# Optimization experiments

Hardware: AMD Instinct MI355X
Metric: run time of the kernel (lower is better)

Reference implementation:

```python
import jax, jax.numpy as jnp
import numpy as np

N_NODES = 100000
N_EDGES = 1600000
IN_DIM = 3
LATENT = 128
LATENT_DEC = 128
NUM_LAYER = 2      # shared-weight middle GCN layers
NUM_LAYER_DEC = 2  # shared-weight middle decoder layers


def _glorot(key, shape):
    fan_in, fan_out = shape[0], shape[1]
    lim = np.sqrt(6.0 / (fan_in + fan_out)).astype(np.float32)
    return jax.random.uniform(key, shape, jnp.float32, -lim, lim)


def setup_inputs() -> dict:
    key = jax.random.key(0)
    ks = jax.random.split(key, 10)
    x = jax.random.normal(ks[0], (N_NODES, IN_DIM), jnp.float32)
    edge_index = jax.random.randint(ks[1], (2, N_EDGES), 0, N_NODES, jnp.int64)
    return {
        "x": x,
        "edge_index": edge_index,
        "W_s": _glorot(ks[2], (IN_DIM, LATENT)),   "b_s": jnp.zeros((LATENT,), jnp.float32),
        "W_m": _glorot(ks[3], (LATENT, LATENT)),   "b_m": jnp.zeros((LATENT,), jnp.float32),
        "W_e": _glorot(ks[4], (LATENT, LATENT)),   "b_e": jnp.zeros((LATENT,), jnp.float32),
        "W_sd": _glorot(ks[5], (LATENT, LATENT_DEC)),    "b_sd": jnp.zeros((LATENT_DEC,), jnp.float32),
        "W_md": _glorot(ks[6], (LATENT_DEC, LATENT_DEC)),"b_md": jnp.zeros((LATENT_DEC,), jnp.float32),
        "W_ed": _glorot(ks[7], (LATENT_DEC, IN_DIM)),    "b_ed": jnp.zeros((IN_DIM,), jnp.float32),
    }


def _gcn_conv(h, W, b, src, dst, dinv):
    # PyG GCNConv: out_i = sum_j norm_ij * (x_j @ W) + b, norm = d^-1/2_i d^-1/2_j
    h = h @ W
    norm = dinv[src] * dinv[dst]                       # [E+N]
    msg = norm[:, None] * h[src]                       # gather + scale
    out = jax.ops.segment_sum(msg, dst, num_segments=N_NODES)  # scatter-add
    return out + b


def reference(x, edge_index, W_s, b_s, W_m, b_m, W_e, b_e, W_sd, b_sd, W_md, b_md, W_ed, b_ed):
    loops = jnp.arange(N_NODES, dtype=edge_index.dtype)
    src = jnp.concatenate([edge_index[0], loops])      # add self-loops
    dst = jnp.concatenate([edge_index[1], loops])
    deg = jax.ops.segment_sum(jnp.ones(src.shape[0], x.dtype), dst, num_segments=N_NODES)
    dinv = jnp.where(deg > 0, jax.lax.rsqrt(deg), 0.0)

    h = jax.nn.relu(_gcn_conv(x, W_s, b_s, src, dst, dinv))
    for _ in range(NUM_LAYER):  # shared weights (ModuleList([layer]*n))
        h = jax.nn.relu(_gcn_conv(h, W_m, b_m, src, dst, dinv))
    h = jax.nn.relu(_gcn_conv(h, W_e, b_e, src, dst, dinv))

    h = jax.nn.relu(h @ W_sd + b_sd)
    for _ in range(NUM_LAYER_DEC):  # shared weights
        h = jax.nn.relu(h @ W_md + b_md)
    y = h @ W_ed + b_ed
    return y + x
```

## Files before the change

### kernel.cpp

```cpp
#include <hip/hip_runtime.h>


typedef __attribute__((ext_vector_type(8))) short short8;
typedef __attribute__((ext_vector_type(4))) float floatx4;
typedef __attribute__((ext_vector_type(2))) float floatx2;

#define BIN_CH 8192
#define NBMAX 512
#define BKT 256
#define HS_STRIDE 68

__device__ __forceinline__ unsigned short f2bf(float f) {
    unsigned int u = __float_as_uint(f);
    u += 0x7fffu + ((u >> 16) & 1u);
    return (unsigned short)(u >> 16);
}
__device__ __forceinline__ unsigned int pk_bf(float a, float b) {
    return (unsigned int)f2bf(a) | ((unsigned int)f2bf(b) << 16);
}
__device__ __forceinline__ unsigned char f2fp8(float f) {
    return (unsigned char)(__builtin_amdgcn_cvt_pk_fp8_f32(f, f, 0, false) & 0xFF);
}
__device__ __forceinline__ short8 ld_frag(const unsigned short* p) {
    uint2 a = *(const uint2*)p;
    uint2 b = *(const uint2*)(p + 4);
    int4 v = make_int4((int)a.x, (int)a.y, (int)b.x, (int)b.y);
    return __builtin_bit_cast(short8, v);
}


__global__ void pack_kernel(const float* __restrict__ W0, const float* __restrict__ W1,
                            const float* __restrict__ W2, const float* __restrict__ W3,
                            unsigned short* __restrict__ P0, unsigned short* __restrict__ P1,
                            unsigned short* __restrict__ P2, unsigned short* __restrict__ P3,
                            int* __restrict__ gfill, unsigned char* __restrict__ t8zrowA,
                            unsigned char* __restrict__ t8zrowB, int NB) {
    if (blockIdx.x == 0) {
        for (int i = threadIdx.x; i < NB; i += 256) gfill[i] = 0;
        if (threadIdx.x < 32) {
            ((unsigned int*)t8zrowA)[threadIdx.x] = 0;
            ((unsigned int*)t8zrowB)[threadIdx.x] = 0;
        }
    }
    int which = blockIdx.x >> 3;
    const float* W = which == 0 ? W0 : which == 1 ? W1 : which == 2 ? W2 : W3;
    unsigned short* P = which == 0 ? P0 : which == 1 ? P1 : which == 2 ? P2 : P3;
    int f = (blockIdx.x & 7) * 256 + threadIdx.x;
    int lane = f & 63, nt = (f >> 6) & 7, kc = f >> 9;
    int kbase = kc * 32 + (lane >> 4) * 8;
    int ncol = nt * 16 + (lane & 15);
    short8 frag;
    #pragma unroll
    for (int j = 0; j < 8; ++j)
        frag[j] = (short)f2bf(W[(size_t)(kbase + j) * 128 + ncol]);
    *((short8*)(P + (size_t)f * 8)) = frag;
}


__global__ __launch_bounds__(512) void bin_kernel(
        const int* __restrict__ src, const int* __restrict__ dst,
        int* __restrict__ gfill, unsigned int* __restrict__ binbuf,
        int NB, int C, int E) {
    __shared__ int h4[4][NBMAX];
    __shared__ int start[NBMAX];
    __shared__ int tot[NBMAX];
    __shared__ int dstoff[NBMAX];
    int tid = threadIdx.x;
    int grp = tid >> 7;
    int e0 = blockIdx.x * BIN_CH;
    for (int i = tid; i < 4 * NBMAX; i += 512) ((int*)h4)[i] = 0;
    __syncthreads();
    for (int i = tid; i < BIN_CH; i += 512) {
        int e = e0 + i;
        if (e < E) atomicAdd(&h4[grp][dst[e] >> 8], 1);
    }
    __syncthreads();
    if (tid < 64) {
        int carry = 0;
        for (int base = 0; base < NB; base += 64) {
            int idx = base + tid;
            int c0 = 0, c1 = 0, c2 = 0, c3 = 0, v = 0;
            if (idx < NB) {
                c0 = h4[0][idx]; c1 = h4[1][idx];
                c2 = h4[2][idx]; c3 = h4[3][idx];
                v = c0 + c1 + c2 + c3;
            }
            int s = v;
            #pragma unroll
            for (int off = 1; off < 64; off <<= 1) {
                int u = __shfl_up(s, off);
                if (tid >= off) s += u;
            }
            if (idx < NB) {
                int ex = carry + s - v;
                start[idx] = ex;
                tot[idx] = v;
                h4[0][idx] = ex;
                h4[1][idx] = ex + c0;
                h4[2][idx] = ex + c0 + c1;
                h4[3][idx] = ex + c0 + c1 + c2;
            }
            carry += __shfl(s, 63);
        }
    }
    __syncthreads();
    for (int i = tid; i < NB; i += 512) {
        int cnt = tot[i];
        int g = cnt ? atomicAdd(&gfill[i], cnt) : 0;
        dstoff[i] = g - start[i];
    }
    __syncthreads();
    for (int i = tid; i < BIN_CH; i += 512) {
        int e = e0 + i;
        if (e >= E) continue;
        int d = dst[e];
        int b = d >> 8;
        int slot = atomicAdd(&h4[grp][b], 1);
        int gidx = b * C + dstoff[b] + slot;
        if (gidx < (b + 1) * C)
            binbuf[gidx] = (unsigned int)src[e] | ((unsigned int)(d & 255) << 17);
    }
}

__global__ __launch_bounds__(256) void build_kernel(
        const unsigned int* __restrict__ binbuf, const int* __restrict__ gfill,
        int* __restrict__ rowptr, float* __restrict__ dinv, int* __restrict__ col,
        int NB, int C, int N, int E) {
    __shared__ int h4[4][BKT];
    __shared__ int hs[BKT];
    __shared__ int tot[BKT];
    __shared__ int bbase_s;
    int b = blockIdx.x, tid = threadIdx.x;
    int grp = tid >> 6;
    int cnt = gfill[b];
    const unsigned int* p = binbuf + (size_t)b * C;
    for (int i = tid; i < 4 * BKT; i += 256) ((int*)h4)[i] = 0;
    __syncthreads();
    if (tid >= 64 && tid < 128) {
        int l = tid - 64;
        int s = 0;
        for (int i = l; i < b; i += 64) s += gfill[i];
        #pragma unroll
        for (int off = 32; off > 0; off >>= 1) s += __shfl_down(s, off);
        if (l == 0) bbase_s = s;
    }
    for (int i = tid; i < cnt; i += 256) atomicAdd(&h4[grp][p[i] >> 17], 1);
    __syncthreads();
    if (tid < 64) {
        int carry = 0;
        for (int base = 0; base < BKT; base += 64) {
            int idx = base + tid;
            int c0 = h4[0][idx], c1 = h4[1][idx], c2 = h4[2][idx], c3 = h4[3][idx];
            int v = c0 + c1 + c2 + c3;
            int s = v;
            #pragma unroll
            for (int off = 1; off < 64; off <<= 1) {
                int u = __shfl_up(s, off);
                if (tid >= off) s += u;
            }
            int ex = carry + s - v;
            hs[idx] = ex;
            tot[idx] = v;
            h4[0][idx] = ex;
            h4[1][idx] = ex + c0;
            h4[2][idx] = ex + c0 + c1;
            h4[3][idx] = ex + c0 + c1 + c2;
            carry += __shfl(s, 63);
        }
    }
    __syncthreads();
    int base = bbase_s;
    if (tid < BKT) {
        int node = b * BKT + tid;
        if (node < N) {
            rowptr[node] = base + hs[tid];
            dinv[node] = 1.0f / sqrtf((float)(tot[tid] + 1));
        }
    }
    if (b == 0 && tid == 0) rowptr[N] = E;
    __syncthreads();
    for (int i = tid; i < cnt; i += 256) {
        unsigned int u = p[i];
        int local = u >> 17;
        int pos = atomicAdd(&h4[grp][local], 1);
        col[base + pos] = (int)(u & 0x1FFFFu);
    }
}


__global__ void in_gemm_kernel(const float* __restrict__ x, const float* __restrict__ W,
                               const float* __restrict__ dinv,
                               unsigned char* __restrict__ t8, int n) {
    int g = blockIdx.x * 256 + threadIdx.x;
    int i = g >> 6, c2 = g & 63;
    if (i >= n) return;
    float x0 = x[i * 3], x1 = x[i * 3 + 1], x2 = x[i * 3 + 2];
    float d = dinv[i];
    int c = c2 * 2;
    float v0 = d * (x0 * W[c]     + x1 * W[128 + c]     + x2 * W[256 + c]);
    float v1 = d * (x0 * W[c + 1] + x1 * W[128 + c + 1] + x2 * W[256 + c + 1]);
    unsigned int pk = __builtin_amdgcn_cvt_pk_fp8_f32(v0, v1, 0, false);
    ((unsigned short*)t8)[(size_t)i * 64 + c2] = (unsigned short)(pk & 0xFFFF);
}


__device__ __forceinline__ void gemm_regs(const short8 af[2][4], const unsigned short* Ws,
                                          int lane, floatx4 acc[2][8]) {
    #pragma unroll
    for (int t = 0; t < 2; ++t)
        #pragma unroll
        for (int nt = 0; nt < 8; ++nt) acc[t][nt] = (floatx4){0.f, 0.f, 0.f, 0.f};
    #pragma unroll
    for (int kc = 0; kc < 4; ++kc) {
        #pragma unroll
        for (int nt = 0; nt < 8; ++nt) {
            short8 bf = *((const short8*)(Ws + ((kc * 8 + nt) * 64 + lane) * 8));
            acc[0][nt] = __builtin_amdgcn_mfma_f32_16x16x32_bf16(af[0][kc], bf, acc[0][nt], 0, 0, 0);
            acc[1][nt] = __builtin_amdgcn_mfma_f32_16x16x32_bf16(af[1][kc], bf, acc[1][nt], 0, 0, 0);
        }
    }
}

__device__ __forceinline__ void gemm_lds(const unsigned short* Hs, const unsigned short* Ws,
                                         int wav, int lane, floatx4 acc[2][8]) {
    int quad = lane >> 4, mrow = lane & 15;
    short8 af[2][4];
    #pragma unroll
    for (int t = 0; t < 2; ++t)
        #pragma unroll
        for (int kc = 0; kc < 4; ++kc)
            af[t][kc] = ld_frag(Hs + (wav * 32 + t * 16 + mrow) * HS_STRIDE + (kc * 4 + quad) * 8);
    gemm_regs(af, Ws, lane, acc);
}

__device__ __forceinline__ void relu_store_hs(
        unsigned short* Hs, const float* __restrict__ bias,
        floatx4 acc[2][8], int wav, int lane) {
    int quad = lane >> 4, mrow = lane & 15;
    #pragma unroll
    for (int t = 0; t < 2; ++t) {
        #pragma unroll
        for (int nt = 0; nt < 8; ++nt) {
            int colc = nt * 16 + mrow;
            float bcol = bias[colc];
            #pragma unroll
            for (int r = 0; r < 4; ++r) {
                int rowl = wav * 32 + t * 16 + quad * 4 + r;
                Hs[rowl * HS_STRIDE + colc] = f2bf(fmaxf(acc[t][nt][r] + bcol, 0.f));
            }
        }
    }
}


__device__ __forceinline__ void agg_to_hs(
        const unsigned char* __restrict__ t8, const int* __restrict__ rowptr,
        const int* __restrict__ col, const float* __restrict__ dinv,
        const float* __restrict__ bias, unsigned short* Hs, int n) {
    int tid = threadIdx.x;
    int lane = tid & 63;
    int q16 = lane >> 4;
    int lq  = lane & 15;
    int oct = (lane >> 3) & 1;
    int l8  = lane & 7;
    int qrow0 = (tid >> 4) * 8;
    const float4* b4 = (const float4*)bias;

    for (int it = 0; it < 8; ++it) {
        int rowl = qrow0 + it;
        int node = blockIdx.x * 128 + rowl;
        if (node >= n) node = n - 1;
        floatx2 acc[8];
        #pragma unroll
        for (int i = 0; i < 8; ++i) acc[i] = (floatx2){0.f, 0.f};

        int beg = rowptr[node];
        int deg = rowptr[node + 1] - beg;
        for (int base = 0; base < deg; base += 32) {
            int m = deg - base;
            int jv0 = (lq < m)      ? col[beg + base + lq]      : n;
            int jv1 = (lq + 16 < m) ? col[beg + base + 16 + lq] : n;
            uint4 v[16];
            #pragma unroll
            for (int q = 0; q < 8; ++q) {
                int j = __shfl(jv0, q16 * 16 + q * 2 + oct);
                v[q] = ((const uint4*)(t8 + (size_t)j * 128))[l8];
            }
            #pragma unroll
            for (int q = 0; q < 8; ++q) {
                int j = __shfl(jv1, q16 * 16 + q * 2 + oct);
                v[8 + q] = ((const uint4*)(t8 + (size_t)j * 128))[l8];
            }
            #pragma unroll
            for (int q = 0; q < 16; ++q) {
                acc[0] += __builtin_amdgcn_cvt_pk_f32_fp8(v[q].x, false);
                acc[1] += __builtin_amdgcn_cvt_pk_f32_fp8(v[q].x, true);
                acc[2] += __builtin_amdgcn_cvt_pk_f32_fp8(v[q].y, false);
                acc[3] += __builtin_amdgcn_cvt_pk_f32_fp8(v[q].y, true);
                acc[4] += __builtin_amdgcn_cvt_pk_f32_fp8(v[q].z, false);
                acc[5] += __builtin_amdgcn_cvt_pk_f32_fp8(v[q].z, true);
                acc[6] += __builtin_amdgcn_cvt_pk_f32_fp8(v[q].w, false);
                acc[7] += __builtin_amdgcn_cvt_pk_f32_fp8(v[q].w, true);
            }
        }
        #pragma unroll
        for (int i = 0; i < 8; ++i) {
            acc[i].x += __shfl_xor(acc[i].x, 8);
            acc[i].y += __shfl_xor(acc[i].y, 8);
        }
        uint4 s = ((const uint4*)(t8 + (size_t)node * 128))[l8];
        acc[0] += __builtin_amdgcn_cvt_pk_f32_fp8(s.x, false);
        acc[1] += __builtin_amdgcn_cvt_pk_f32_fp8(s.x, true);
        acc[2] += __builtin_amdgcn_cvt_pk_f32_fp8(s.y, false);
        acc[3] += __builtin_amdgcn_cvt_pk_f32_fp8(s.y, true);
        acc[4] += __builtin_amdgcn_cvt_pk_f32_fp8(s.z, false);
        acc[5] += __builtin_amdgcn_cvt_pk_f32_fp8(s.z, true);
        acc[6] += __builtin_amdgcn_cvt_pk_f32_fp8(s.w, false);
        acc[7] += __builtin_amdgcn_cvt_pk_f32_fp8(s.w, true);

        float di = dinv[node];
        float o[16];
        #pragma unroll
        for (int k = 0; k < 4; ++k) {
            float4 bb = b4[l8 * 4 + k];
            o[k*4+0] = fmaxf(di * acc[k*2].x   + bb.x, 0.f);
            o[k*4+1] = fmaxf(di * acc[k*2].y   + bb.y, 0.f);
            o[k*4+2] = fmaxf(di * acc[k*2+1].x + bb.z, 0.f);
            o[k*4+3] = fmaxf(di * acc[k*2+1].y + bb.w, 0.f);
        }
        if (oct == 0) {
            unsigned short* hp = Hs + rowl * HS_STRIDE + l8 * 16;
            uint2 w;
            w.x = pk_bf(o[0],  o[1]);  w.y = pk_bf(o[2],  o[3]);
            *(uint2*)(hp)     = w;
            w.x = pk_bf(o[4],  o[5]);  w.y = pk_bf(o[6],  o[7]);
            *(uint2*)(hp + 4) = w;
            w.x = pk_bf(o[8],  o[9]);  w.y = pk_bf(o[10], o[11]);
            *(uint2*)(hp + 8) = w;
            w.x = pk_bf(o[12], o[13]); w.y = pk_bf(o[14], o[15]);
            *(uint2*)(hp + 12) = w;
        }
    }
}


__global__ __launch_bounds__(256, 3) void agg_gemm_kernel(
        const unsigned char* __restrict__ t8, const int* __restrict__ rowptr,
        const int* __restrict__ col, const float* __restrict__ dinv,
        const float* __restrict__ bias, const unsigned short* __restrict__ Wp,
        unsigned char* __restrict__ outp, int n) {
    __shared__ unsigned short Hs[128 * HS_STRIDE];
    agg_to_hs(t8, rowptr, col, dinv, bias, Hs, n);

    int tid = threadIdx.x;
    int wav = tid >> 6, lane = tid & 63;
    int quad = lane >> 4, mrow = lane & 15;
    int row0 = blockIdx.x * 128 + wav * 32;

    floatx4 acc[2][8];
    gemm_lds(Hs, Wp, wav, lane, acc);

    #pragma unroll
    for (int t = 0; t < 2; ++t) {
        int rbase = row0 + t * 16 + quad * 4;
        float dv[4];
        #pragma unroll
        for (int r = 0; r < 4; ++r)
            dv[r] = (rbase + r < n) ? dinv[rbase + r] : 0.f;
        #pragma unroll
        for (int nt = 0; nt < 8; ++nt) {
            int colc = nt * 16 + mrow;
            #pragma unroll
            for (int r = 0; r < 4; ++r) {
                int row = rbase + r;
                if (row < n)
                    outp[(size_t)row * 128 + colc] = f2fp8(acc[t][nt][r] * dv[r]);
            }
        }
    }
}


__global__ __launch_bounds__(256, 3) void agg_dec_kernel(
        const unsigned char* __restrict__ t8, const int* __restrict__ rowptr,
        const int* __restrict__ col, const float* __restrict__ dinv,
        const float* __restrict__ bias,
        const unsigned short* __restrict__ Wp_sd, const float* __restrict__ b_sd,
        const unsigned short* __restrict__ Wp_md, const float* __restrict__ b_md,
        const float* __restrict__ W_ed, const float* __restrict__ b_ed,
        const float* __restrict__ x, float* __restrict__ out, int n) {
    __shared__ unsigned short Hs[128 * HS_STRIDE];
    agg_to_hs(t8, rowptr, col, dinv, bias, Hs, n);

    int tid = threadIdx.x;
    int wav = tid >> 6, lane = tid & 63;
    int quad = lane >> 4, mrow = lane & 15;
    int row0 = blockIdx.x * 128 + wav * 32;

    floatx4 acc[2][8];
    gemm_lds(Hs, Wp_sd, wav, lane, acc);
    relu_store_hs(Hs, b_sd, acc, wav, lane);
    gemm_lds(Hs, Wp_md, wav, lane, acc);
    relu_store_hs(Hs, b_md, acc, wav, lane);
    gemm_lds(Hs, Wp_md, wav, lane, acc);

    float wed[8][3];
    #pragma unroll
    for (int nt = 0; nt < 8; ++nt) {
        int c = nt * 16 + mrow;
        #pragma unroll
        for (int k = 0; k < 3; ++k) wed[nt][k] = W_ed[c * 3 + k];
    }
    #pragma unroll
    for (int t = 0; t < 2; ++t) {
        #pragma unroll
        for (int r = 0; r < 4; ++r) {
            float s0 = 0.f, s1 = 0.f, s2 = 0.f;
            #pragma unroll
            for (int nt = 0; nt < 8; ++nt) {
                float v = fmaxf(acc[t][nt][r] + b_md[nt * 16 + mrow], 0.f);
                s0 += v * wed[nt][0]; s1 += v * wed[nt][1]; s2 += v * wed[nt][2];
            }
            #pragma unroll
            for (int off = 1; off < 16; off <<= 1) {
                s0 += __shfl_xor(s0, off);
                s1 += __shfl_xor(s1, off);
                s2 += __shfl_xor(s2, off);
            }
            if (mrow == 0) {
                int row = row0 + t * 16 + quad * 4 + r;
                if (row < n) {
                    out[row * 3 + 0] = s0 + b_ed[0] + x[row * 3 + 0];
                    out[row * 3 + 1] = s1 + b_ed[1] + x[row * 3 + 1];
                    out[row * 3 + 2] = s2 + b_ed[2] + x[row * 3 + 2];
                }
            }
        }
    }
}


extern "C" void kernel_launch(void* const* d_in, const int* in_sizes, int n_in,
                              void* d_out, int out_size, void* d_ws, size_t ws_size,
                              hipStream_t stream) {
    const float* x    = (const float*)d_in[0];
    const int*   ei   = (const int*)d_in[1];
    const float* W_s  = (const float*)d_in[2];
    const float* b_s  = (const float*)d_in[3];
    const float* W_m  = (const float*)d_in[4];
    const float* b_m  = (const float*)d_in[5];
    const float* W_e  = (const float*)d_in[6];
    const float* b_e  = (const float*)d_in[7];
    const float* W_sd = (const float*)d_in[8];
    const float* b_sd = (const float*)d_in[9];
    const float* W_md = (const float*)d_in[10];
    const float* b_md = (const float*)d_in[11];
    const float* W_ed = (const float*)d_in[12];
    const float* b_ed = (const float*)d_in[13];
    float* outp = (float*)d_out;

    const int N = in_sizes[0] / 3;
    const int E = in_sizes[1] / 2;
    const int* src = ei;
    const int* dst = ei + E;

    const int NB = (N + BKT - 1) / BKT;
    const int C  = (((E / NB) * 3 / 2) + 255) & ~255;

    char* p = (char*)d_ws;
    auto carve = [&](size_t bytes) {
        void* r = (void*)p;
        p += (bytes + 255) & ~(size_t)255;
        return r;
    };
    int*   rowptr = (int*)  carve((size_t)(N + 1) * 4);
    int*   col    = (int*)  carve((size_t)E * 4);
    float* dinv   = (float*)carve((size_t)N * 4);
    int*   gfill  = (int*)  carve((size_t)NB * 4);
    unsigned int* binbuf = (unsigned int*)carve((size_t)NB * C * 4);
    unsigned short* Wp_m  = (unsigned short*)carve(16384 * 2);
    unsigned short* Wp_e  = (unsigned short*)carve(16384 * 2);
    unsigned short* Wp_sd = (unsigned short*)carve(16384 * 2);
    unsigned short* Wp_md = (unsigned short*)carve(16384 * 2);
    unsigned char*  T8a = (unsigned char*) carve((size_t)(N + 1) * 128);
    unsigned char*  T8b = (unsigned char*) carve((size_t)(N + 1) * 128);
    (void)ws_size;

    const int gBin = (E + BIN_CH - 1) / BIN_CH;
    const int gRow128 = (N + 127) / 128;

    pack_kernel<<<32, 256, 0, stream>>>(W_m, W_e, W_sd, W_md, Wp_m, Wp_e, Wp_sd, Wp_md,
                                        gfill, T8a + (size_t)N * 128,
                                        T8b + (size_t)N * 128, NB);

    bin_kernel<<<gBin, 512, 0, stream>>>(src, dst, gfill, binbuf, NB, C, E);
    build_kernel<<<NB, 256, 0, stream>>>(binbuf, gfill, rowptr, dinv, col, NB, C, N, E);

    in_gemm_kernel<<<(N * 64 + 255) / 256, 256, 0, stream>>>(x, W_s, dinv, T8a, N);
    agg_gemm_kernel<<<gRow128, 256, 0, stream>>>(T8a, rowptr, col, dinv, b_s, Wp_m, T8b, N);
    agg_gemm_kernel<<<gRow128, 256, 0, stream>>>(T8b, rowptr, col, dinv, b_m, Wp_m, T8a, N);
    agg_gemm_kernel<<<gRow128, 256, 0, stream>>>(T8a, rowptr, col, dinv, b_m, Wp_e, T8b, N);

    agg_dec_kernel<<<gRow128, 256, 0, stream>>>(T8b, rowptr, col, dinv, b_e,
                                                Wp_sd, b_sd, Wp_md, b_md,
                                                W_ed, b_ed, x, outp, N);
}
```

Baseline: 372.9 us.

## Use 512-thread blocks and prefetch next node's neighbor indices during aggregation

Blocks grow from 256 to 512 threads, so each wave handles 16 rows of the MFMA GEMM instead of 32 and each thread group aggregates 4 nodes instead of 8. The aggregation loop now loads rowptr for all of its nodes up front, issues the self-loop feature load early, and fetches the next node's column indices while the current node's gathers are in flight. Launch bounds move to (512,4). The goal is more waves per CU and better hiding of gather latency, at the cost of register pressure and a second MFMA pass per row tile being lost.

```diff
diff --git a/kernel.cpp b/kernel.cpp
--- a/kernel.cpp
+++ b/kernel.cpp
@@ -204,50 +204,42 @@
 }
 
 
-__device__ __forceinline__ void gemm_regs(const short8 af[2][4], const unsigned short* Ws,
-                                          int lane, floatx4 acc[2][8]) {
-    #pragma unroll
-    for (int t = 0; t < 2; ++t)
-        #pragma unroll
-        for (int nt = 0; nt < 8; ++nt) acc[t][nt] = (floatx4){0.f, 0.f, 0.f, 0.f};
+__device__ __forceinline__ void gemm_regs16(const short8 af[4], const unsigned short* Ws,
+                                            int lane, floatx4 acc[8]) {
+    #pragma unroll
+    for (int nt = 0; nt < 8; ++nt) acc[nt] = (floatx4){0.f, 0.f, 0.f, 0.f};
     #pragma unroll
     for (int kc = 0; kc < 4; ++kc) {
         #pragma unroll
         for (int nt = 0; nt < 8; ++nt) {
             short8 bf = *((const short8*)(Ws + ((kc * 8 + nt) * 64 + lane) * 8));
-            acc[0][nt] = __builtin_amdgcn_mfma_f32_16x16x32_bf16(af[0][kc], bf, acc[0][nt], 0, 0, 0);
-            acc[1][nt] = __builtin_amdgcn_mfma_f32_16x16x32_bf16(af[1][kc], bf, acc[1][nt], 0, 0, 0);
-        }
-    }
-}
-
-__device__ __forceinline__ void gemm_lds(const unsigned short* Hs, const unsigned short* Ws,
-                                         int wav, int lane, floatx4 acc[2][8]) {
+            acc[nt] = __builtin_amdgcn_mfma_f32_16x16x32_bf16(af[kc], bf, acc[nt], 0, 0, 0);
+        }
+    }
+}
+
+__device__ __forceinline__ void gemm_lds16(const unsigned short* Hs, const unsigned short* Ws,
+                                           int wav, int lane, floatx4 acc[8]) {
     int quad = lane >> 4, mrow = lane & 15;
-    short8 af[2][4];
-    #pragma unroll
-    for (int t = 0; t < 2; ++t)
-        #pragma unroll
-        for (int kc = 0; kc < 4; ++kc)
-            af[t][kc] = ld_frag(Hs + (wav * 32 + t * 16 + mrow) * HS_STRIDE + (kc * 4 + quad) * 8);
-    gemm_regs(af, Ws, lane, acc);
-}
-
-__device__ __forceinline__ void relu_store_hs(
+    short8 af[4];
+    #pragma unroll
+    for (int kc = 0; kc < 4; ++kc)
+        af[kc] = ld_frag(Hs + (wav * 16 + mrow) * HS_STRIDE + (kc * 4 + quad) * 8);
+    gemm_regs16(af, Ws, lane, acc);
+}
+
+__device__ __forceinline__ void relu_store_hs16(
         unsigned short* Hs, const float* __restrict__ bias,
-        floatx4 acc[2][8], int wav, int lane) {
+        floatx4 acc[8], int wav, int lane) {
     int quad = lane >> 4, mrow = lane & 15;
     #pragma unroll
-    for (int t = 0; t < 2; ++t) {
-        #pragma unroll
-        for (int nt = 0; nt < 8; ++nt) {
-            int colc = nt * 16 + mrow;
-            float bcol = bias[colc];
-            #pragma unroll
-            for (int r = 0; r < 4; ++r) {
-                int rowl = wav * 32 + t * 16 + quad * 4 + r;
-                Hs[rowl * HS_STRIDE + colc] = f2bf(fmaxf(acc[t][nt][r] + bcol, 0.f));
-            }
+    for (int nt = 0; nt < 8; ++nt) {
+        int colc = nt * 16 + mrow;
+        float bcol = bias[colc];
+        #pragma unroll
+        for (int r = 0; r < 4; ++r) {
+            int rowl = wav * 16 + quad * 4 + r;
+            Hs[rowl * HS_STRIDE + colc] = f2bf(fmaxf(acc[nt][r] + bcol, 0.f));
         }
     }
 }
@@ -263,32 +255,69 @@
     int lq  = lane & 15;
     int oct = (lane >> 3) & 1;
     int l8  = lane & 7;
-    int qrow0 = (tid >> 4) * 8;
+    int qrow0 = (tid >> 4) * 4;
     const float4* b4 = (const float4*)bias;
 
-    for (int it = 0; it < 8; ++it) {
+    int nd0 = blockIdx.x * 128 + qrow0;
+    int bg[4], dg[4];
+    #pragma unroll
+    for (int it = 0; it < 4; ++it) {
+        int node = nd0 + it; if (node >= n) node = n - 1;
+        bg[it] = rowptr[node];
+        dg[it] = rowptr[node + 1] - bg[it];
+    }
+    int jv0 = (lq < dg[0])      ? col[bg[0] + lq]      : n;
+    int jv1 = (lq + 16 < dg[0]) ? col[bg[0] + 16 + lq] : n;
+
+    for (int it = 0; it < 4; ++it) {
         int rowl = qrow0 + it;
-        int node = blockIdx.x * 128 + rowl;
-        if (node >= n) node = n - 1;
+        int node = nd0 + it; if (node >= n) node = n - 1;
         floatx2 acc[8];
         #pragma unroll
         for (int i = 0; i < 8; ++i) acc[i] = (floatx2){0.f, 0.f};
 
-        int beg = rowptr[node];
-        int deg = rowptr[node + 1] - beg;
-        for (int base = 0; base < deg; base += 32) {
+        uint4 s = ((const uint4*)(t8 + (size_t)node * 128))[l8];
+
+        int deg = dg[it];
+        uint4 v[16];
+        #pragma unroll
+        for (int q = 0; q < 8; ++q) {
+            int j = __shfl(jv0, q16 * 16 + q * 2 + oct);
+            v[q] = ((const uint4*)(t8 + (size_t)j * 128))[l8];
+        }
+        #pragma unroll
+        for (int q = 0; q < 8; ++q) {
+            int j = __shfl(jv1, q16 * 16 + q * 2 + oct);
+            v[8 + q] = ((const uint4*)(t8 + (size_t)j * 128))[l8];
+        }
+        int njv0 = n, njv1 = n;
+        if (it < 3) {
+            njv0 = (lq < dg[it + 1])      ? col[bg[it + 1] + lq]      : n;
+            njv1 = (lq + 16 < dg[it + 1]) ? col[bg[it + 1] + 16 + lq] : n;
+        }
+        #pragma unroll
+        for (int q = 0; q < 16; ++q) {
+            acc[0] += __builtin_amdgcn_cvt_pk_f32_fp8(v[q].x, false);
+            acc[1] += __builtin_amdgcn_cvt_pk_f32_fp8(v[q].x, true);
+            acc[2] += __builtin_amdgcn_cvt_pk_f32_fp8(v[q].y, false);
+            acc[3] += __builtin_amdgcn_cvt_pk_f32_fp8(v[q].y, true);
+            acc[4] += __builtin_amdgcn_cvt_pk_f32_fp8(v[q].z, false);
+            acc[5] += __builtin_amdgcn_cvt_pk_f32_fp8(v[q].z, true);
+            acc[6] += __builtin_amdgcn_cvt_pk_f32_fp8(v[q].w, false);
+            acc[7] += __builtin_amdgcn_cvt_pk_f32_fp8(v[q].w, true);
+        }
+        for (int base = 32; base < deg; base += 32) {
             int m = deg - base;
-            int jv0 = (lq < m)      ? col[beg + base + lq]      : n;
-            int jv1 = (lq + 16 < m) ? col[beg + base + 16 + lq] : n;
-            uint4 v[16];
+            int a0 = (lq < m)      ? col[bg[it] + base + lq]      : n;
+            int a1 = (lq + 16 < m) ? col[bg[it] + base + 16 + lq] : n;
             #pragma unroll
             for (int q = 0; q < 8; ++q) {
-                int j = __shfl(jv0, q16 * 16 + q * 2 + oct);
+                int j = __shfl(a0, q16 * 16 + q * 2 + oct);
                 v[q] = ((const uint4*)(t8 + (size_t)j * 128))[l8];
             }
             #pragma unroll
             for (int q = 0; q < 8; ++q) {
-                int j = __shfl(jv1, q16 * 16 + q * 2 + oct);
+                int j = __shfl(a1, q16 * 16 + q * 2 + oct);
                 v[8 + q] = ((const uint4*)(t8 + (size_t)j * 128))[l8];
             }
             #pragma unroll
@@ -308,7 +337,6 @@
             acc[i].x += __shfl_xor(acc[i].x, 8);
             acc[i].y += __shfl_xor(acc[i].y, 8);
         }
-        uint4 s = ((const uint4*)(t8 + (size_t)node * 128))[l8];
         acc[0] += __builtin_amdgcn_cvt_pk_f32_fp8(s.x, false);
         acc[1] += __builtin_amdgcn_cvt_pk_f32_fp8(s.x, true);
         acc[2] += __builtin_amdgcn_cvt_pk_f32_fp8(s.y, false);
@@ -332,19 +360,20 @@
             unsigned short* hp = Hs + rowl * HS_STRIDE + l8 * 16;
             uint2 w;
             w.x = pk_bf(o[0],  o[1]);  w.y = pk_bf(o[2],  o[3]);
-            *(uint2*)(hp)     = w;
+            *(uint2*)(hp)      = w;
             w.x = pk_bf(o[4],  o[5]);  w.y = pk_bf(o[6],  o[7]);
-            *(uint2*)(hp + 4) = w;
+            *(uint2*)(hp + 4)  = w;
             w.x = pk_bf(o[8],  o[9]);  w.y = pk_bf(o[10], o[11]);
-            *(uint2*)(hp + 8) = w;
+            *(uint2*)(hp + 8)  = w;
             w.x = pk_bf(o[12], o[13]); w.y = pk_bf(o[14], o[15]);
             *(uint2*)(hp + 12) = w;
         }
-    }
-}
-
-
-__global__ __launch_bounds__(256, 3) void agg_gemm_kernel(
+        jv0 = njv0; jv1 = njv1;
+    }
+}
+
+
+__global__ __launch_bounds__(512, 4) void agg_gemm_kernel(
         const unsigned char* __restrict__ t8, const int* __restrict__ rowptr,
         const int* __restrict__ col, const float* __restrict__ dinv,
         const float* __restrict__ bias, const unsigned short* __restrict__ Wp,
@@ -355,33 +384,30 @@
     int tid = threadIdx.x;
     int wav = tid >> 6, lane = tid & 63;
     int quad = lane >> 4, mrow = lane & 15;
-    int row0 = blockIdx.x * 128 + wav * 32;
-
-    floatx4 acc[2][8];
-    gemm_lds(Hs, Wp, wav, lane, acc);
-
-    #pragma unroll
-    for (int t = 0; t < 2; ++t) {
-        int rbase = row0 + t * 16 + quad * 4;
-        float dv[4];
-        #pragma unroll
-        for (int r = 0; r < 4; ++r)
-            dv[r] = (rbase + r < n) ? dinv[rbase + r] : 0.f;
-        #pragma unroll
-        for (int nt = 0; nt < 8; ++nt) {
-            int colc = nt * 16 + mrow;
-            #pragma unroll
-            for (int r = 0; r < 4; ++r) {
-                int row = rbase + r;
-                if (row < n)
-                    outp[(size_t)row * 128 + colc] = f2fp8(acc[t][nt][r] * dv[r]);
-            }
-        }
-    }
-}
-
-
-__global__ __launch_bounds__(256, 3) void agg_dec_kernel(
+    int row0 = blockIdx.x * 128 + wav * 16;
+
+    floatx4 acc[8];
+    gemm_lds16(Hs, Wp, wav, lane, acc);
+
+    int rbase = row0 + quad * 4;
+    float dv[4];
+    #pragma unroll
+    for (int r = 0; r < 4; ++r)
+        dv[r] = (rbase + r < n) ? dinv[rbase + r] : 0.f;
+    #pragma unroll
+    for (int nt = 0; nt < 8; ++nt) {
+        int colc = nt * 16 + mrow;
+        #pragma unroll
+        for (int r = 0; r < 4; ++r) {
+            int row = rbase + r;
+            if (row < n)
+                outp[(size_t)row * 128 + colc] = f2fp8(acc[nt][r] * dv[r]);
+        }
+    }
+}
+
+
+__global__ __launch_bounds__(512, 4) void agg_dec_kernel(
         const unsigned char* __restrict__ t8, const int* __restrict__ rowptr,
         const int* __restrict__ col, const float* __restrict__ dinv,
         const float* __restrict__ bias,
@@ -395,14 +421,14 @@
     int tid = threadIdx.x;
     int wav = tid >> 6, lane = tid & 63;
     int quad = lane >> 4, mrow = lane & 15;
-    int row0 = blockIdx.x * 128 + wav * 32;
-
-    floatx4 acc[2][8];
-    gemm_lds(Hs, Wp_sd, wav, lane, acc);
-    relu_store_hs(Hs, b_sd, acc, wav, lane);
-    gemm_lds(Hs, Wp_md, wav, lane, acc);
-    relu_store_hs(Hs, b_md, acc, wav, lane);
-    gemm_lds(Hs, Wp_md, wav, lane, acc);
+    int row0 = blockIdx.x * 128 + wav * 16;
+
+    floatx4 acc[8];
+    gemm_lds16(Hs, Wp_sd, wav, lane, acc);
+    relu_store_hs16(Hs, b_sd, acc, wav, lane);
+    gemm_lds16(Hs, Wp_md, wav, lane, acc);
+    relu_store_hs16(Hs, b_md, acc, wav, lane);
+    gemm_lds16(Hs, Wp_md, wav, lane, acc);
 
     float wed[8][3];
     #pragma unroll
@@ -412,28 +438,25 @@
         for (int k = 0; k < 3; ++k) wed[nt][k] = W_ed[c * 3 + k];
     }
     #pragma unroll
-    for (int t = 0; t < 2; ++t) {
-        #pragma unroll
-        for (int r = 0; r < 4; ++r) {
-            float s0 = 0.f, s1 = 0.f, s2 = 0.f;
-            #pragma unroll
-            for (int nt = 0; nt < 8; ++nt) {
-                float v = fmaxf(acc[t][nt][r] + b_md[nt * 16 + mrow], 0.f);
-                s0 += v * wed[nt][0]; s1 += v * wed[nt][1]; s2 += v * wed[nt][2];
-            }
-            #pragma unroll
-            for (int off = 1; off < 16; off <<= 1) {
-                s0 += __shfl_xor(s0, off);
-                s1 += __shfl_xor(s1, off);
-                s2 += __shfl_xor(s2, off);
-            }
-            if (mrow == 0) {
-                int row = row0 + t * 16 + quad * 4 + r;
-                if (row < n) {
-                    out[row * 3 + 0] = s0 + b_ed[0] + x[row * 3 + 0];
-                    out[row * 3 + 1] = s1 + b_ed[1] + x[row * 3 + 1];
-                    out[row * 3 + 2] = s2 + b_ed[2] + x[row * 3 + 2];
-                }
+    for (int r = 0; r < 4; ++r) {
+        float s0 = 0.f, s1 = 0.f, s2 = 0.f;
+        #pragma unroll
+        for (int nt = 0; nt < 8; ++nt) {
+            float v = fmaxf(acc[nt][r] + b_md[nt * 16 + mrow], 0.f);
+            s0 += v * wed[nt][0]; s1 += v * wed[nt][1]; s2 += v * wed[nt][2];
+        }
+        #pragma unroll
+        for (int off = 1; off < 16; off <<= 1) {
+            s0 += __shfl_xor(s0, off);
+            s1 += __shfl_xor(s1, off);
+            s2 += __shfl_xor(s2, off);
+        }
+        if (mrow == 0) {
+            int row = row0 + quad * 4 + r;
+            if (row < n) {
+                out[row * 3 + 0] = s0 + b_ed[0] + x[row * 3 + 0];
+                out[row * 3 + 1] = s1 + b_ed[1] + x[row * 3 + 1];
+                out[row * 3 + 2] = s2 + b_ed[2] + x[row * 3 + 2];
             }
         }
     }
@@ -497,11 +520,11 @@
     build_kernel<<<NB, 256, 0, stream>>>(binbuf, gfill, rowptr, dinv, col, NB, C, N, E);
 
     in_gemm_kernel<<<(N * 64 + 255) / 256, 256, 0, stream>>>(x, W_s, dinv, T8a, N);
-    agg_gemm_kernel<<<gRow128, 256, 0, stream>>>(T8a, rowptr, col, dinv, b_s, Wp_m, T8b, N);
-    agg_gemm_kernel<<<gRow128, 256, 0, stream>>>(T8b, rowptr, col, dinv, b_m, Wp_m, T8a, N);
-    agg_gemm_kernel<<<gRow128, 256, 0, stream>>>(T8a, rowptr, col, dinv, b_m, Wp_e, T8b, N);
-
-    agg_dec_kernel<<<gRow128, 256, 0, stream>>>(T8b, rowptr, col, dinv, b_e,
+    agg_gemm_kernel<<<gRow128, 512, 0, stream>>>(T8a, rowptr, col, dinv, b_s, Wp_m, T8b, N);
+    agg_gemm_kernel<<<gRow128, 512, 0, stream>>>(T8b, rowptr, col, dinv, b_m, Wp_m, T8a, N);
+    agg_gemm_kernel<<<gRow128, 512, 0, stream>>>(T8a, rowptr, col, dinv, b_m, Wp_e, T8b, N);
+
+    agg_dec_kernel<<<gRow128, 512, 0, stream>>>(T8b, rowptr, col, dinv, b_e,
                                                 Wp_sd, b_sd, Wp_md, b_md,
                                                 W_ed, b_ed, x, outp, N);
 }
```

Measured after the change: 392.4 us. 5.2% more time.

## Split final aggregation from decoder into separate agg and decoder kernels

Applied to the files above, without the earlier changes.

The last GCN aggregation is no longer fused into the decoder. A standalone agg_kernel (16 nodes per block) writes a bf16 activation buffer to global memory, and a new decoder_kernel loads A-fragments straight from that buffer into registers for the first GEMM. The aim is to give the latency-bound gather its own launch shape and occupancy, and to let the decoder run at a higher occupancy bound. The cost is an extra kernel launch and a round trip of about 25 MB of bf16 activations through global memory.

```diff
diff --git a/kernel.cpp b/kernel.cpp
--- a/kernel.cpp
+++ b/kernel.cpp
@@ -204,6 +204,88 @@
 }
 
 
+__global__ __launch_bounds__(256) void agg_kernel(
+        const unsigned char* __restrict__ t8, const int* __restrict__ rowptr,
+        const int* __restrict__ col, const float* __restrict__ dinv,
+        const float* __restrict__ bias, unsigned short* __restrict__ out, int n) {
+    int node = blockIdx.x * 16 + (threadIdx.x >> 4);
+    int lane = threadIdx.x & 63;
+    int q16 = lane >> 4;
+    int lq  = lane & 15;
+    int oct = (lane >> 3) & 1;
+    int l8  = lane & 7;
+    if (node >= n) node = n - 1;
+    floatx2 acc[8];
+    #pragma unroll
+    for (int i = 0; i < 8; ++i) acc[i] = (floatx2){0.f, 0.f};
+
+    int beg = rowptr[node];
+    int deg = rowptr[node + 1] - beg;
+    for (int base = 0; base < deg; base += 32) {
+        int m = deg - base;
+        int jv0 = (lq < m)      ? col[beg + base + lq]      : n;
+        int jv1 = (lq + 16 < m) ? col[beg + base + 16 + lq] : n;
+        uint4 v[16];
+        #pragma unroll
+        for (int q = 0; q < 8; ++q) {
+            int j = __shfl(jv0, q16 * 16 + q * 2 + oct);
+            v[q] = ((const uint4*)(t8 + (size_t)j * 128))[l8];
+        }
+        #pragma unroll
+        for (int q = 0; q < 8; ++q) {
+            int j = __shfl(jv1, q16 * 16 + q * 2 + oct);
+            v[8 + q] = ((const uint4*)(t8 + (size_t)j * 128))[l8];
+        }
+        #pragma unroll
+        for (int q = 0; q < 16; ++q) {
+            acc[0] += __builtin_amdgcn_cvt_pk_f32_fp8(v[q].x, false);
+            acc[1] += __builtin_amdgcn_cvt_pk_f32_fp8(v[q].x, true);
+            acc[2] += __builtin_amdgcn_cvt_pk_f32_fp8(v[q].y, false);
+            acc[3] += __builtin_amdgcn_cvt_pk_f32_fp8(v[q].y, true);
+            acc[4] += __builtin_amdgcn_cvt_pk_f32_fp8(v[q].z, false);
+            acc[5] += __builtin_amdgcn_cvt_pk_f32_fp8(v[q].z, true);
+            acc[6] += __builtin_amdgcn_cvt_pk_f32_fp8(v[q].w, false);
+            acc[7] += __builtin_amdgcn_cvt_pk_f32_fp8(v[q].w, true);
+        }
+    }
+    #pragma unroll
+    for (int i = 0; i < 8; ++i) {
+        acc[i].x += __shfl_xor(acc[i].x, 8);
+        acc[i].y += __shfl_xor(acc[i].y, 8);
+    }
+    uint4 s = ((const uint4*)(t8 + (size_t)node * 128))[l8];
+    acc[0] += __builtin_amdgcn_cvt_pk_f32_fp8(s.x, false);
+    acc[1] += __builtin_amdgcn_cvt_pk_f32_fp8(s.x, true);
+    acc[2] += __builtin_amdgcn_cvt_pk_f32_fp8(s.y, false);
+    acc[3] += __builtin_amdgcn_cvt_pk_f32_fp8(s.y, true);
+    acc[4] += __builtin_amdgcn_cvt_pk_f32_fp8(s.z, false);
+    acc[5] += __builtin_amdgcn_cvt_pk_f32_fp8(s.z, true);
+    acc[6] += __builtin_amdgcn_cvt_pk_f32_fp8(s.w, false);
+    acc[7] += __builtin_amdgcn_cvt_pk_f32_fp8(s.w, true);
+
+    float di = dinv[node];
+    const float4* b4 = (const float4*)bias;
+    float o[16];
+    #pragma unroll
+    for (int k = 0; k < 4; ++k) {
+        float4 bb = b4[l8 * 4 + k];
+        o[k*4+0] = fmaxf(di * acc[k*2].x   + bb.x, 0.f);
+        o[k*4+1] = fmaxf(di * acc[k*2].y   + bb.y, 0.f);
+        o[k*4+2] = fmaxf(di * acc[k*2+1].x + bb.z, 0.f);
+        o[k*4+3] = fmaxf(di * acc[k*2+1].y + bb.w, 0.f);
+    }
+    if (oct == 0) {
+        uint4 w0, w1;
+        w0.x = pk_bf(o[0],  o[1]);  w0.y = pk_bf(o[2],  o[3]);
+        w0.z = pk_bf(o[4],  o[5]);  w0.w = pk_bf(o[6],  o[7]);
+        w1.x = pk_bf(o[8],  o[9]);  w1.y = pk_bf(o[10], o[11]);
+        w1.z = pk_bf(o[12], o[13]); w1.w = pk_bf(o[14], o[15]);
+        ((uint4*)(out + (size_t)node * 128))[l8 * 2]     = w0;
+        ((uint4*)(out + (size_t)node * 128))[l8 * 2 + 1] = w1;
+    }
+}
+
+
 __device__ __forceinline__ void gemm_regs(const short8 af[2][4], const unsigned short* Ws,
                                           int lane, floatx4 acc[2][8]) {
     #pragma unroll
@@ -332,11 +414,11 @@
             unsigned short* hp = Hs + rowl * HS_STRIDE + l8 * 16;
             uint2 w;
             w.x = pk_bf(o[0],  o[1]);  w.y = pk_bf(o[2],  o[3]);
-            *(uint2*)(hp)     = w;
+            *(uint2*)(hp)      = w;
             w.x = pk_bf(o[4],  o[5]);  w.y = pk_bf(o[6],  o[7]);
-            *(uint2*)(hp + 4) = w;
+            *(uint2*)(hp + 4)  = w;
             w.x = pk_bf(o[8],  o[9]);  w.y = pk_bf(o[10], o[11]);
-            *(uint2*)(hp + 8) = w;
+            *(uint2*)(hp + 8)  = w;
             w.x = pk_bf(o[12], o[13]); w.y = pk_bf(o[14], o[15]);
             *(uint2*)(hp + 12) = w;
         }
@@ -381,24 +463,30 @@
 }
 
 
-__global__ __launch_bounds__(256, 3) void agg_dec_kernel(
-        const unsigned char* __restrict__ t8, const int* __restrict__ rowptr,
-        const int* __restrict__ col, const float* __restrict__ dinv,
-        const float* __restrict__ bias,
+__global__ __launch_bounds__(256, 4) void decoder_kernel(
+        const unsigned short* __restrict__ A,
         const unsigned short* __restrict__ Wp_sd, const float* __restrict__ b_sd,
         const unsigned short* __restrict__ Wp_md, const float* __restrict__ b_md,
         const float* __restrict__ W_ed, const float* __restrict__ b_ed,
         const float* __restrict__ x, float* __restrict__ out, int n) {
     __shared__ unsigned short Hs[128 * HS_STRIDE];
-    agg_to_hs(t8, rowptr, col, dinv, bias, Hs, n);
-
     int tid = threadIdx.x;
     int wav = tid >> 6, lane = tid & 63;
     int quad = lane >> 4, mrow = lane & 15;
     int row0 = blockIdx.x * 128 + wav * 32;
 
+    short8 af[2][4];
+    #pragma unroll
+    for (int t = 0; t < 2; ++t) {
+        int arow = row0 + t * 16 + mrow; if (arow >= n) arow = n - 1;
+        const unsigned short* abase = A + (size_t)arow * 128 + quad * 8;
+        #pragma unroll
+        for (int kc = 0; kc < 4; ++kc)
+            af[t][kc] = *((const short8*)(abase + kc * 32));
+    }
+
     floatx4 acc[2][8];
-    gemm_lds(Hs, Wp_sd, wav, lane, acc);
+    gemm_regs(af, Wp_sd, lane, acc);
     relu_store_hs(Hs, b_sd, acc, wav, lane);
     gemm_lds(Hs, Wp_md, wav, lane, acc);
     relu_store_hs(Hs, b_md, acc, wav, lane);
@@ -484,10 +572,12 @@
     unsigned short* Wp_md = (unsigned short*)carve(16384 * 2);
     unsigned char*  T8a = (unsigned char*) carve((size_t)(N + 1) * 128);
     unsigned char*  T8b = (unsigned char*) carve((size_t)(N + 1) * 128);
+    unsigned short* A   = (unsigned short*)carve((size_t)N * 128 * 2);
     (void)ws_size;
 
     const int gBin = (E + BIN_CH - 1) / BIN_CH;
     const int gRow128 = (N + 127) / 128;
+    const int gNode16 = (N + 15) / 16;
 
     pack_kernel<<<32, 256, 0, stream>>>(W_m, W_e, W_sd, W_md, Wp_m, Wp_e, Wp_sd, Wp_md,
                                         gfill, T8a + (size_t)N * 128,
@@ -501,7 +591,7 @@
     agg_gemm_kernel<<<gRow128, 256, 0, stream>>>(T8b, rowptr, col, dinv, b_m, Wp_m, T8a, N);
     agg_gemm_kernel<<<gRow128, 256, 0, stream>>>(T8a, rowptr, col, dinv, b_m, Wp_e, T8b, N);
 
-    agg_dec_kernel<<<gRow128, 256, 0, stream>>>(T8b, rowptr, col, dinv, b_e,
-                                                Wp_sd, b_sd, Wp_md, b_md,
+    agg_kernel<<<gNode16, 256, 0, stream>>>(T8b, rowptr, col, dinv, b_e, A, N);
+    decoder_kernel<<<gRow128, 256, 0, stream>>>(A, Wp_sd, b_sd, Wp_md, b_md,
                                                 W_ed, b_ed, x, outp, N);
 }
```

Measured after the change: 362.3 us. 1.03x faster.
